# Optimization experiments

Hardware: AMD Instinct MI355X
Metric: run time of the kernel (lower is better)

Reference implementation:

```python
import jax, jax.numpy as jnp
import numpy as np

N = 50000       # nodes
E = 800000      # raw edges (self-loops added in reference, per PyG GATConv default)
F_IN = 256      # input feature dim (dataset.num_features stand-in)
H = 4           # heads (layer 1)
C = 32          # hidden_channels per head
CLS = 16        # num_classes (layer 2 out, heads=1)


def setup_inputs() -> dict:
    key = jax.random.key(0)
    ks = jax.random.split(key, 12)
    s = 0.05
    return {
        "x": jax.random.normal(ks[0], (N, F_IN), jnp.float32),
        "edge_index": jax.random.randint(ks[1], (2, E), 0, N, dtype=jnp.int64),
        "W1": jax.random.normal(ks[2], (F_IN, H * C), jnp.float32) * s,
        "att_src1": jax.random.normal(ks[3], (H, C), jnp.float32) * s,
        "att_dst1": jax.random.normal(ks[4], (H, C), jnp.float32) * s,
        "b1": jnp.zeros((H * C,), jnp.float32),
        "W2": jax.random.normal(ks[5], (H * C, CLS), jnp.float32) * s,
        "att_src2": jax.random.normal(ks[6], (1, CLS), jnp.float32) * s,
        "att_dst2": jax.random.normal(ks[7], (1, CLS), jnp.float32) * s,
        "b2": jnp.zeros((CLS,), jnp.float32),
    }


def gat_conv(x, src, dst, W, a_src, a_dst, b, heads, ch):
    """One GATConv (concat=True). src/dst include self-loops."""
    n = x.shape[0]
    h = (x @ W).reshape(n, heads, ch)                       # [N,H,C]
    alpha_s = jnp.sum(h * a_src, axis=-1)                   # [N,H]
    alpha_d = jnp.sum(h * a_dst, axis=-1)                   # [N,H]
    e = jax.nn.leaky_relu(alpha_s[src] + alpha_d[dst], 0.2) # [E',H]
    # segment softmax over incoming edges of each destination node
    m = jax.ops.segment_max(e, dst, num_segments=n)         # [N,H]
    ex = jnp.exp(e - m[dst])
    den = jax.ops.segment_sum(ex, dst, num_segments=n)      # [N,H]
    coef = ex / (den[dst] + 1e-16)                          # [E',H]
    # weighted scatter-aggregate of source features
    out = jax.ops.segment_sum(h[src] * coef[:, :, None], dst, num_segments=n)
    return out.reshape(n, heads * ch) + b


def reference(x, edge_index, W1, att_src1, att_dst1, b1, W2, att_src2, att_dst2, b2):
    n = x.shape[0]
    loop = jnp.arange(n, dtype=edge_index.dtype)
    src = jnp.concatenate([edge_index[0], loop])
    dst = jnp.concatenate([edge_index[1], loop])
    # eval mode: F.dropout is identity
    h = gat_conv(x, src, dst, W1, att_src1, att_dst1, b1, H, C)
    h = jax.nn.elu(h)
    out = gat_conv(h, src, dst, W2, att_src2, att_dst2, b2, 1, CLS)
    return out
```

## Files before the change

kernel.cpp:

```cpp
#include <hip/hip_runtime.h>
#include <hip/hip_bf16.h>
#include <math.h>

#define NNODES 50000
#define FIN 256
#define HH 4
#define CC 32
#define D1 128
#define CLS 16
#define NBUCK ((NNODES + 255) >> 8)
#define CHUNK 4096

typedef __attribute__((ext_vector_type(8))) short bfrag8;
typedef __attribute__((ext_vector_type(4))) float facc4;

__device__ __forceinline__ float lrelu(float x){ return x > 0.f ? x : 0.2f*x; }

__device__ __forceinline__ unsigned short f2bu(float x){
  __hip_bfloat16 h = __float2bfloat16(x);
  return *reinterpret_cast<unsigned short*>(&h);
}
__device__ __forceinline__ unsigned int pbf(float a, float b){
  return (unsigned int)f2bu(a) | ((unsigned int)f2bu(b) << 16);
}
__device__ __forceinline__ float2 bf2x(unsigned int u){
  float2 r;
  r.x = __uint_as_float(u << 16);
  r.y = __uint_as_float(u & 0xffff0000u);
  return r;
}

__global__ void wprep_kernel(const float* __restrict__ W, unsigned short* __restrict__ Wt) {
  int t = blockIdx.x*256 + threadIdx.x;
  if (t >= FIN*D1) return;
  int k = t >> 7, c = t & 127;
  Wt[c*FIN + k] = f2bu(W[t]);
}

__global__ __launch_bounds__(256) void gemm1_mfma(const float* __restrict__ x,
                                                  const unsigned int* __restrict__ Wt,
                                                  unsigned int* __restrict__ h1b) {
  __shared__ unsigned int Bs[128*256/2];
  __shared__ unsigned int As[64*64/2];
  int tid = threadIdx.x;
  int wv = tid >> 6, lane = tid & 63;
  int r0 = blockIdx.x * 64;

  for (int it = 0; it < 16; it++) {
    int w16 = it*256 + tid;
    int c = w16 >> 5, k8 = w16 & 31;
    uint4 v = ((const uint4*)Wt)[w16];
    int byt = (c*512 + k8*16) ^ ((c&7)<<4);
    *(uint4*)((char*)Bs + byt) = v;
  }

  facc4 acc[8];
  #pragma unroll
  for (int t=0;t<8;t++) acc[t] = (facc4){0.f,0.f,0.f,0.f};

  int arow = tid >> 2, apart = tid & 3;
  int mrow = lane & 15, kb = lane >> 4;

  for (int stage = 0; stage < 4; stage++) {
    int gr = r0 + arow;
    const float* src = x + (size_t)gr*FIN + stage*64 + apart*16;
    float4 f0, f1, f2, f3;
    if (gr < NNODES) {
      f0 = *(const float4*)(src);
      f1 = *(const float4*)(src+4);
      f2 = *(const float4*)(src+8);
      f3 = *(const float4*)(src+12);
    } else {
      f0 = f1 = f2 = f3 = make_float4(0.f,0.f,0.f,0.f);
    }
    uint4 u0, u1;
    u0.x = pbf(f0.x,f0.y); u0.y = pbf(f0.z,f0.w);
    u0.z = pbf(f1.x,f1.y); u0.w = pbf(f1.z,f1.w);
    u1.x = pbf(f2.x,f2.y); u1.y = pbf(f2.z,f2.w);
    u1.z = pbf(f3.x,f3.y); u1.w = pbf(f3.z,f3.w);
    __syncthreads();
    int b0 = (arow*128 + apart*32) ^ ((arow&7)<<4);
    int b1 = (arow*128 + apart*32 + 16) ^ ((arow&7)<<4);
    *(uint4*)((char*)As + b0) = u0;
    *(uint4*)((char*)As + b1) = u1;
    __syncthreads();
    #pragma unroll
    for (int ks = 0; ks < 2; ks++) {
      int row = wv*16 + mrow;
      int abyt = (row*128 + ks*64 + kb*16) ^ ((row&7)<<4);
      bfrag8 afrag = *(bfrag8*)((char*)As + abyt);
      #pragma unroll
      for (int ct = 0; ct < 8; ct++) {
        int c = ct*16 + mrow;
        int bbyt = (c*512 + stage*128 + ks*64 + kb*16) ^ ((c&7)<<4);
        bfrag8 bfrag = *(bfrag8*)((char*)Bs + bbyt);
        acc[ct] = __builtin_amdgcn_mfma_f32_16x16x32_bf16(afrag, bfrag, acc[ct], 0, 0, 0);
      }
    }
  }
  int orow0 = r0 + wv*16 + (lane>>4)*4;
  int ocol = lane & 15;
  #pragma unroll
  for (int r=0; r<4; r++) {
    int gr = orow0 + r;
    if (gr < NNODES) {
      #pragma unroll
      for (int ct=0; ct<4; ct++)
        h1b[(size_t)gr*64 + ct*16 + ocol] = pbf(acc[ct][r], acc[ct+4][r]);
    }
  }
}

__global__ void alpha1_kernel(const unsigned int* __restrict__ h1b,
                              const float* __restrict__ asrc,
                              const float* __restrict__ adst,
                              float* __restrict__ as1, float* __restrict__ ad1) {
  int t = blockIdx.x * blockDim.x + threadIdx.x;
  if (t >= NNODES*HH) return;
  int i = t >> 2, h = t & 3;
  const unsigned int* base = h1b + (size_t)i*64 + (h&1)*32;
  const float* ap = asrc + h*CC;
  const float* bp = adst + h*CC;
  bool hi = (h >= 2);
  float s=0.f, d=0.f;
  #pragma unroll
  for (int q8=0; q8<8; q8++){
    uint4 u = *(const uint4*)(base + q8*4);
    float v0 = hi ? bf2x(u.x).y : bf2x(u.x).x;
    float v1 = hi ? bf2x(u.y).y : bf2x(u.y).x;
    float v2 = hi ? bf2x(u.z).y : bf2x(u.z).x;
    float v3 = hi ? bf2x(u.w).y : bf2x(u.w).x;
    int q = q8*4;
    s = fmaf(v0, ap[q+0], s); d = fmaf(v0, bp[q+0], d);
    s = fmaf(v1, ap[q+1], s); d = fmaf(v1, bp[q+1], d);
    s = fmaf(v2, ap[q+2], s); d = fmaf(v2, bp[q+2], d);
    s = fmaf(v3, ap[q+3], s); d = fmaf(v3, bp[q+3], d);
  }
  as1[t] = s; ad1[t] = d;
}

__global__ __launch_bounds__(256) void bucket_count_kernel(const int* __restrict__ dsts,
                                                           int* __restrict__ bcnt, int E) {
  __shared__ int cnt[NBUCK];
  for (int t=threadIdx.x; t<NBUCK; t+=256) cnt[t]=0;
  __syncthreads();
  int base = blockIdx.x*CHUNK, lim = min(base+CHUNK, E);
  for (int e = base+threadIdx.x; e < lim; e += 256)
    atomicAdd(&cnt[dsts[e]>>8], 1);
  __syncthreads();
  for (int t=threadIdx.x; t<NBUCK; t+=256)
    if (cnt[t]) atomicAdd(&bcnt[t], cnt[t]);
}

__global__ __launch_bounds__(256) void bucket_scan_kernel(const int* __restrict__ bcnt,
                                                          int* __restrict__ gstart,
                                                          int* __restrict__ gcur) {
  int t = threadIdx.x;
  int orig = (t < NBUCK) ? bcnt[t] : 0;
  int v = orig;
  int ln = t & 63, wv = t >> 6;
  #pragma unroll
  for (int off=1; off<64; off<<=1){ int u=__shfl_up(v,off,64); if(ln>=off) v+=u; }
  __shared__ int wsum[4], wbase[4];
  if (ln==63) wsum[wv]=v;
  __syncthreads();
  if (t==0){
    int s=0;
    for(int k=0;k<4;k++){ wbase[k]=s; s+=wsum[k]; }
  }
  __syncthreads();
  int incl = wbase[wv]+v;
  if (t < NBUCK){ gstart[t+1]=incl; gcur[t]=incl-orig; }
  if (t==0) gstart[0]=0;
}

__global__ __launch_bounds__(256) void bin_kernel(const int* __restrict__ srcs,
                                                  const int* __restrict__ dsts,
                                                  int* __restrict__ gcur,
                                                  unsigned int* __restrict__ binned, int E) {
  __shared__ int cnt[NBUCK];
  __shared__ int rbase[NBUCK];
  for (int t=threadIdx.x; t<NBUCK; t+=256) cnt[t]=0;
  __syncthreads();
  int base = blockIdx.x*CHUNK, lim = min(base+CHUNK, E);
  for (int e = base+threadIdx.x; e < lim; e += 256)
    atomicAdd(&cnt[dsts[e]>>8], 1);
  __syncthreads();
  for (int t=threadIdx.x; t<NBUCK; t+=256){
    rbase[t] = cnt[t] ? atomicAdd(&gcur[t], cnt[t]) : 0;
    cnt[t] = 0;
  }
  __syncthreads();
  for (int e = base+threadIdx.x; e < lim; e += 256){
    int d = dsts[e], s = srcs[e];
    int b = d >> 8;
    int p = rbase[b] + atomicAdd(&cnt[b], 1);
    binned[p] = ((unsigned int)s << 8) | (unsigned int)(d & 255);
  }
}

__global__ __launch_bounds__(256) void bucketcsr_kernel(const int* __restrict__ gstart,
                                                        const unsigned int* __restrict__ binned,
                                                        int* __restrict__ offs,
                                                        unsigned short* __restrict__ srcsort, int E) {
  int b = blockIdx.x;
  int s0 = gstart[b], s1 = gstart[b+1];
  int t = threadIdx.x;
  __shared__ int cnt[256];
  __shared__ int cur[256];
  cnt[t] = 0;
  __syncthreads();
  for (int j = s0+t; j < s1; j += 256)
    atomicAdd(&cnt[binned[j] & 255], 1);
  __syncthreads();
  int orig = cnt[t], v = orig;
  int ln = t & 63, wv = t >> 6;
  #pragma unroll
  for (int off=1; off<64; off<<=1){ int u=__shfl_up(v,off,64); if(ln>=off) v+=u; }
  __shared__ int wsum[4], wbase[4];
  if (ln==63) wsum[wv]=v;
  __syncthreads();
  if (t==0){
    int s=0;
    for(int k=0;k<4;k++){ wbase[k]=s; s+=wsum[k]; }
  }
  __syncthreads();
  int excl = wbase[wv] + v - orig;
  cur[t] = excl;
  int node = b*256 + t;
  if (node < NNODES) offs[node] = s0 + excl;
  if (node == NNODES-1) offs[NNODES] = E;
  __syncthreads();
  for (int j = s0+t; j < s1; j += 256){
    unsigned int e = binned[j];
    int p = s0 + atomicAdd(&cur[e & 255], 1);
    srcsort[p] = (unsigned short)(e >> 8);
  }
}

__global__ __launch_bounds__(256) void agg1_kernel(
    const unsigned int* __restrict__ h1b, const float* __restrict__ as1,
    const float* __restrict__ ad1, const int* __restrict__ offs,
    const unsigned short* __restrict__ srcsort, const float* __restrict__ b1,
    float* __restrict__ out1) {
  __shared__ float exs[4][4][64];
  __shared__ int   ss [4][64];
  int warp = threadIdx.x >> 6;
  int lane = threadIdx.x & 63;
  int i = blockIdx.x * 4 + warp;
  if (i >= NNODES) return;
  int start = offs[i], end = offs[i+1];
  float4 adv = *(const float4*)(ad1 + (size_t)i*4);
  float4 asv = *(const float4*)(as1 + (size_t)i*4);
  float ad[4] = {adv.x, adv.y, adv.z, adv.w};
  float wself[4];
  {
    float av[4] = {asv.x, asv.y, asv.z, asv.w};
    #pragma unroll
    for (int h=0;h<4;h++) wself[h] = expf(lrelu(av[h] + ad[h]));
  }
  int hlo = lane >> 5, hhi = hlo + 2;
  float den[4] = {0.f, 0.f, 0.f, 0.f};
  float accA, accB;
  {
    float2 hv = bf2x(h1b[(size_t)i*64 + lane]);
    accA = wself[hlo] * hv.x; accB = wself[hhi] * hv.y;
  }
  for (int c0 = start; c0 < end; c0 += 64) {
    int cnt = min(64, end - c0);
    int j = c0 + lane;
    if (j < end) {
      int s = (int)srcsort[j];
      float4 a = *(const float4*)(as1 + (size_t)s*4);
      float e0 = expf(lrelu(a.x + ad[0]));
      float e1 = expf(lrelu(a.y + ad[1]));
      float e2 = expf(lrelu(a.z + ad[2]));
      float e3 = expf(lrelu(a.w + ad[3]));
      den[0] += e0; den[1] += e1; den[2] += e2; den[3] += e3;
      exs[warp][0][lane] = e0; exs[warp][1][lane] = e1;
      exs[warp][2][lane] = e2; exs[warp][3][lane] = e3;
      ss[warp][lane] = s;
    }
    #pragma unroll 2
    for (int j2 = 0; j2 < cnt; j2++) {
      int s = ss[warp][j2];
      float2 hv = bf2x(h1b[(size_t)s*64 + lane]);
      accA = fmaf(exs[warp][hlo][j2], hv.x, accA);
      accB = fmaf(exs[warp][hhi][j2], hv.y, accB);
    }
  }
  #pragma unroll
  for (int off=1; off<64; off<<=1) {
    #pragma unroll
    for (int h=0;h<4;h++) den[h] += __shfl_xor(den[h], off, 64);
  }
  float invlo = 1.f / (den[hlo] + wself[hlo] + 1e-16f);
  float invhi = 1.f / (den[hhi] + wself[hhi] + 1e-16f);
  float v0 = accA * invlo + b1[lane];
  float v1 = accB * invhi + b1[lane + 64];
  out1[(size_t)i*D1 + lane]      = v0 > 0.f ? v0 : expm1f(v0);
  out1[(size_t)i*D1 + 64 + lane] = v1 > 0.f ? v1 : expm1f(v1);
}

__global__ __launch_bounds__(256) void layer2_proj_kernel(
    const float* __restrict__ out1, const float* __restrict__ W2,
    const float* __restrict__ asrc2, const float* __restrict__ adst2,
    __hip_bfloat16* __restrict__ h2b, float* __restrict__ as2, float* __restrict__ ad2) {
  __shared__ float w_s[D1*CLS];
  for (int l = threadIdx.x; l < D1*CLS; l += 256) w_s[l] = W2[l];
  __syncthreads();
  int warp = threadIdx.x >> 6, lane = threadIdx.x & 63;
  int i = blockIdx.x*4 + warp;
  if (i >= NNODES) return;
  int c = lane & 15, kq = lane >> 4;
  float acc = 0.f;
  const float* xp = out1 + (size_t)i*D1 + kq*32;
  #pragma unroll
  for (int q=0; q<8; q++) {
    float4 v = *(const float4*)(xp + q*4);
    int k = kq*32 + q*4;
    acc = fmaf(v.x, w_s[(k+0)*CLS + c], acc);
    acc = fmaf(v.y, w_s[(k+1)*CLS + c], acc);
    acc = fmaf(v.z, w_s[(k+2)*CLS + c], acc);
    acc = fmaf(v.w, w_s[(k+3)*CLS + c], acc);
  }
  acc += __shfl_xor(acc, 16, 64);
  acc += __shfl_xor(acc, 32, 64);
  if (lane < 16) h2b[(size_t)i*CLS + c] = __float2bfloat16(acc);
  float s = acc * asrc2[c];
  float d = acc * adst2[c];
  #pragma unroll
  for (int off=1; off<16; off<<=1) { s += __shfl_xor(s, off, 64); d += __shfl_xor(d, off, 64); }
  if (lane == 0) { as2[i] = s; ad2[i] = d; }
}

__global__ __launch_bounds__(256) void agg2_kernel(
    const unsigned int* __restrict__ h2b, const float* __restrict__ as2,
    const float* __restrict__ ad2, const int* __restrict__ offs,
    const unsigned short* __restrict__ srcsort, const float* __restrict__ b2,
    float* __restrict__ out) {
  int warp = threadIdx.x >> 6, lane = threadIdx.x & 63;
  int i = blockIdx.x*4 + warp;
  if (i >= NNODES) return;
  int start = offs[i], end = offs[i+1];
  float ad = ad2[i];
  float wself = expf(lrelu(as2[i] + ad));
  int g = lane >> 3, cp = lane & 7;
  float2 acc = make_float2(0.f, 0.f);
  float denp = 0.f;
  if (g == 0) {
    float2 hv = bf2x(h2b[(size_t)i*(CLS/2) + cp]);
    acc.x = wself*hv.x; acc.y = wself*hv.y;
    denp = wself;
  }
  for (int j = start + g; j < end; j += 8) {
    int s = (int)srcsort[j];
    float w = expf(lrelu(as2[s] + ad));
    denp += w;
    float2 hv = bf2x(h2b[(size_t)s*(CLS/2) + cp]);
    acc.x = fmaf(w, hv.x, acc.x);
    acc.y = fmaf(w, hv.y, acc.y);
  }
  #pragma unroll
  for (int off=8; off<64; off<<=1) {
    acc.x += __shfl_xor(acc.x, off, 64);
    acc.y += __shfl_xor(acc.y, off, 64);
    denp  += __shfl_xor(denp,  off, 64);
  }
  if (lane < 8) {
    float inv = 1.f / (denp + 1e-16f);
    float2 o;
    o.x = acc.x * inv + b2[2*cp];
    o.y = acc.y * inv + b2[2*cp+1];
    *(float2*)(out + (size_t)i*CLS + 2*cp) = o;
  }
}

extern "C" void kernel_launch(void* const* d_in, const int* in_sizes, int n_in,
                              void* d_out, int out_size, void* d_ws, size_t ws_size,
                              hipStream_t stream) {
  const float* x     = (const float*)d_in[0];
  const int*   eidx  = (const int*)d_in[1];
  const float* W1    = (const float*)d_in[2];
  const float* asrc1 = (const float*)d_in[3];
  const float* adst1 = (const float*)d_in[4];
  const float* b1    = (const float*)d_in[5];
  const float* W2    = (const float*)d_in[6];
  const float* asrc2 = (const float*)d_in[7];
  const float* adst2 = (const float*)d_in[8];
  const float* b2    = (const float*)d_in[9];
  float* out = (float*)d_out;

  const int E = in_sizes[1] / 2;
  const int* srcs = eidx;
  const int* dsts = eidx + E;
  const int EBLK = (E + CHUNK - 1) / CHUNK;

  char* ws = (char*)d_ws;
  size_t off = 0;
  auto alloc = [&](size_t bytes) -> void* {
    void* p = ws + off;
    off = (off + bytes + 255) & ~(size_t)255;
    return p;
  };
  unsigned int*   h1b     = (unsigned int*)alloc((size_t)NNODES*(D1/2)*4);
  float*          out1    = (float*)alloc((size_t)NNODES*D1*4);
  unsigned short* Wt      = (unsigned short*)alloc((size_t)FIN*D1*2);
  float*          as1     = (float*)alloc((size_t)NNODES*HH*4);
  float*          ad1     = (float*)alloc((size_t)NNODES*HH*4);
  __hip_bfloat16* h2b     = (__hip_bfloat16*)alloc((size_t)NNODES*CLS*2);
  float*          as2     = (float*)alloc((size_t)NNODES*4);
  float*          ad2     = (float*)alloc((size_t)NNODES*4);
  int*            bcnt    = (int*)alloc((size_t)NBUCK*4);
  int*            gstart  = (int*)alloc((size_t)(NBUCK+1)*4);
  int*            gcur    = (int*)alloc((size_t)NBUCK*4);
  int*            offs    = (int*)alloc((size_t)(NNODES+1)*4);
  unsigned int*   binned  = (unsigned int*)alloc((size_t)E*4);
  unsigned short* srcsort = (unsigned short*)alloc((size_t)E*2);

  (void)hipMemsetAsync(bcnt, 0, (size_t)NBUCK*4, stream);

  wprep_kernel<<<(FIN*D1+255)/256, 256, 0, stream>>>(W1, Wt);
  gemm1_mfma<<<(NNODES+63)/64, 256, 0, stream>>>(x, (const unsigned int*)Wt, h1b);
  alpha1_kernel<<<(NNODES*HH+255)/256, 256, 0, stream>>>(h1b, asrc1, adst1, as1, ad1);

  bucket_count_kernel<<<EBLK, 256, 0, stream>>>(dsts, bcnt, E);
  bucket_scan_kernel<<<1, 256, 0, stream>>>(bcnt, gstart, gcur);
  bin_kernel<<<EBLK, 256, 0, stream>>>(srcs, dsts, gcur, binned, E);
  bucketcsr_kernel<<<NBUCK, 256, 0, stream>>>(gstart, binned, offs, srcsort, E);

  agg1_kernel<<<(NNODES+3)/4, 256, 0, stream>>>(h1b, as1, ad1, offs, srcsort, b1, out1);

  layer2_proj_kernel<<<(NNODES+3)/4, 256, 0, stream>>>(out1, W2, asrc2, adst2, h2b, as2, ad2);
  agg2_kernel<<<(NNODES+3)/4, 256, 0, stream>>>((const unsigned int*)h2b, as2, ad2, offs, srcsort, b2, out);
}
```

Baseline: 162.6 us.

## Store layer-1 output as packed bf16, use fast exp2 and deeper unrolling

The intermediate layer-1 activation is now written as packed bf16 pairs, which halves the write traffic in agg1 and the read traffic in layer2_proj. The projection kernel unpacks the lo/hi halves to match the interleaved head layout. expf and expm1f are replaced by a hardware exp2-based fast exp, and the gather loops in agg1 and agg2 are unrolled further to keep more loads in flight. This trades some accuracy (bf16 intermediate, approximate exp, exp-1 near zero) for less memory traffic and cheaper math.

New measurement: 158.5 us. -2.5%, faster.

```diff
diff --git a/kernel.cpp b/kernel.cpp
--- a/kernel.cpp
+++ b/kernel.cpp
@@ -15,6 +15,14 @@
 typedef __attribute__((ext_vector_type(4))) float facc4;
 
 __device__ __forceinline__ float lrelu(float x){ return x > 0.f ? x : 0.2f*x; }
+
+__device__ __forceinline__ float fexp(float x){
+#if __has_builtin(__builtin_amdgcn_exp2f)
+  return __builtin_amdgcn_exp2f(x * 1.4426950408889634f);
+#else
+  return exp2f(x * 1.4426950408889634f);
+#endif
+}
 
 __device__ __forceinline__ unsigned short f2bu(float x){
   __hip_bfloat16 h = __float2bfloat16(x);
@@ -242,7 +250,7 @@
     const unsigned int* __restrict__ h1b, const float* __restrict__ as1,
     const float* __restrict__ ad1, const int* __restrict__ offs,
     const unsigned short* __restrict__ srcsort, const float* __restrict__ b1,
-    float* __restrict__ out1) {
+    unsigned int* __restrict__ out1p) {
   __shared__ float exs[4][4][64];
   __shared__ int   ss [4][64];
   int warp = threadIdx.x >> 6;
@@ -257,7 +265,7 @@
   {
     float av[4] = {asv.x, asv.y, asv.z, asv.w};
     #pragma unroll
-    for (int h=0;h<4;h++) wself[h] = expf(lrelu(av[h] + ad[h]));
+    for (int h=0;h<4;h++) wself[h] = fexp(lrelu(av[h] + ad[h]));
   }
   int hlo = lane >> 5, hhi = hlo + 2;
   float den[4] = {0.f, 0.f, 0.f, 0.f};
@@ -272,16 +280,16 @@
     if (j < end) {
       int s = (int)srcsort[j];
       float4 a = *(const float4*)(as1 + (size_t)s*4);
-      float e0 = expf(lrelu(a.x + ad[0]));
-      float e1 = expf(lrelu(a.y + ad[1]));
-      float e2 = expf(lrelu(a.z + ad[2]));
-      float e3 = expf(lrelu(a.w + ad[3]));
+      float e0 = fexp(lrelu(a.x + ad[0]));
+      float e1 = fexp(lrelu(a.y + ad[1]));
+      float e2 = fexp(lrelu(a.z + ad[2]));
+      float e3 = fexp(lrelu(a.w + ad[3]));
       den[0] += e0; den[1] += e1; den[2] += e2; den[3] += e3;
       exs[warp][0][lane] = e0; exs[warp][1][lane] = e1;
       exs[warp][2][lane] = e2; exs[warp][3][lane] = e3;
       ss[warp][lane] = s;
     }
-    #pragma unroll 2
+    #pragma unroll 8
     for (int j2 = 0; j2 < cnt; j2++) {
       int s = ss[warp][j2];
       float2 hv = bf2x(h1b[(size_t)s*64 + lane]);
@@ -298,12 +306,13 @@
   float invhi = 1.f / (den[hhi] + wself[hhi] + 1e-16f);
   float v0 = accA * invlo + b1[lane];
   float v1 = accB * invhi + b1[lane + 64];
-  out1[(size_t)i*D1 + lane]      = v0 > 0.f ? v0 : expm1f(v0);
-  out1[(size_t)i*D1 + 64 + lane] = v1 > 0.f ? v1 : expm1f(v1);
+  v0 = v0 > 0.f ? v0 : fexp(v0) - 1.f;
+  v1 = v1 > 0.f ? v1 : fexp(v1) - 1.f;
+  out1p[(size_t)i*64 + lane] = pbf(v0, v1);
 }
 
 __global__ __launch_bounds__(256) void layer2_proj_kernel(
-    const float* __restrict__ out1, const float* __restrict__ W2,
+    const unsigned int* __restrict__ out1p, const float* __restrict__ W2,
     const float* __restrict__ asrc2, const float* __restrict__ adst2,
     __hip_bfloat16* __restrict__ h2b, float* __restrict__ as2, float* __restrict__ ad2) {
   __shared__ float w_s[D1*CLS];
@@ -313,16 +322,22 @@
   int i = blockIdx.x*4 + warp;
   if (i >= NNODES) return;
   int c = lane & 15, kq = lane >> 4;
+  const unsigned int* xp = out1p + (size_t)i*64 + (kq&1)*32;
+  bool hi = kq >= 2;
+  int kb = (kq&1)*32 + (hi ? 64 : 0);
   float acc = 0.f;
-  const float* xp = out1 + (size_t)i*D1 + kq*32;
-  #pragma unroll
-  for (int q=0; q<8; q++) {
-    float4 v = *(const float4*)(xp + q*4);
-    int k = kq*32 + q*4;
-    acc = fmaf(v.x, w_s[(k+0)*CLS + c], acc);
-    acc = fmaf(v.y, w_s[(k+1)*CLS + c], acc);
-    acc = fmaf(v.z, w_s[(k+2)*CLS + c], acc);
-    acc = fmaf(v.w, w_s[(k+3)*CLS + c], acc);
+  #pragma unroll
+  for (int q8=0; q8<8; q8++) {
+    uint4 u = *(const uint4*)(xp + q8*4);
+    float v0 = hi ? bf2x(u.x).y : bf2x(u.x).x;
+    float v1 = hi ? bf2x(u.y).y : bf2x(u.y).x;
+    float v2 = hi ? bf2x(u.z).y : bf2x(u.z).x;
+    float v3 = hi ? bf2x(u.w).y : bf2x(u.w).x;
+    int k = kb + q8*4;
+    acc = fmaf(v0, w_s[(k+0)*CLS + c], acc);
+    acc = fmaf(v1, w_s[(k+1)*CLS + c], acc);
+    acc = fmaf(v2, w_s[(k+2)*CLS + c], acc);
+    acc = fmaf(v3, w_s[(k+3)*CLS + c], acc);
   }
   acc += __shfl_xor(acc, 16, 64);
   acc += __shfl_xor(acc, 32, 64);
@@ -344,7 +359,7 @@
   if (i >= NNODES) return;
   int start = offs[i], end = offs[i+1];
   float ad = ad2[i];
-  float wself = expf(lrelu(as2[i] + ad));
+  float wself = fexp(lrelu(as2[i] + ad));
   int g = lane >> 3, cp = lane & 7;
   float2 acc = make_float2(0.f, 0.f);
   float denp = 0.f;
@@ -353,9 +368,10 @@
     acc.x = wself*hv.x; acc.y = wself*hv.y;
     denp = wself;
   }
+  #pragma unroll 4
   for (int j = start + g; j < end; j += 8) {
     int s = (int)srcsort[j];
-    float w = expf(lrelu(as2[s] + ad));
+    float w = fexp(lrelu(as2[s] + ad));
     denp += w;
     float2 hv = bf2x(h2b[(size_t)s*(CLS/2) + cp]);
     acc.x = fmaf(w, hv.x, acc.x);
@@ -404,7 +420,7 @@
     return p;
   };
   unsigned int*   h1b     = (unsigned int*)alloc((size_t)NNODES*(D1/2)*4);
-  float*          out1    = (float*)alloc((size_t)NNODES*D1*4);
+  unsigned int*   out1p   = (unsigned int*)alloc((size_t)NNODES*(D1/2)*4);
   unsigned short* Wt      = (unsigned short*)alloc((size_t)FIN*D1*2);
   float*          as1     = (float*)alloc((size_t)NNODES*HH*4);
   float*          ad1     = (float*)alloc((size_t)NNODES*HH*4);
@@ -429,8 +445,8 @@
   bin_kernel<<<EBLK, 256, 0, stream>>>(srcs, dsts, gcur, binned, E);
   bucketcsr_kernel<<<NBUCK, 256, 0, stream>>>(gstart, binned, offs, srcsort, E);
 
-  agg1_kernel<<<(NNODES+3)/4, 256, 0, stream>>>(h1b, as1, ad1, offs, srcsort, b1, out1);
-
-  layer2_proj_kernel<<<(NNODES+3)/4, 256, 0, stream>>>(out1, W2, asrc2, adst2, h2b, as2, ad2);
+  agg1_kernel<<<(NNODES+3)/4, 256, 0, stream>>>(h1b, as1, ad1, offs, srcsort, b1, out1p);
+
+  layer2_proj_kernel<<<(NNODES+3)/4, 256, 0, stream>>>(out1p, W2, asrc2, adst2, h2b, as2, ad2);
   agg2_kernel<<<(NNODES+3)/4, 256, 0, stream>>>((const unsigned int*)h2b, as2, ad2, offs, srcsort, b2, out);
 }
```
